# Kernel tuning notes

Measured on AMD Instinct MI355X. Metric: run time of the kernel, lower is better.

The kernel has to match this reference:

```python
import jax, jax.numpy as jnp
import numpy as np


def _layer_norm(x, g, b, eps=1e-5):
    mu = x.mean(-1, keepdims=True)
    var = ((x - mu) ** 2).mean(-1, keepdims=True)
    return (x - mu) * jax.lax.rsqrt(var + eps) * g + b


def _linear(x, w, b):
    # torch nn.Linear: y = x @ W^T + b, w has shape (out, in)
    return jnp.einsum('...i,oi->...o', x, w) + b


def setup_inputs() -> dict:
    key = jax.random.key(0)
    ks = jax.random.split(key, 12)
    B, N, C = 1, 512, 128
    s = 0.02  # weight init scale
    f32 = jnp.float32
    return {
        'X': jax.random.normal(ks[0], (B, N, N, C), f32),
        'mask': jax.random.randint(ks[1], (B, N, N, 1), 0, 2) > 0,
        # first LayerNorm
        'ln1_g': jnp.ones((C,), f32), 'ln1_b': jnp.zeros((C,), f32),
        # left edge MLP: Linear -> Sigmoid -> Linear
        'lw1': jax.random.normal(ks[2], (C, C), f32) * s, 'lb1': jnp.zeros((C,), f32),
        'lw2': jax.random.normal(ks[3], (C, C), f32) * s, 'lb2': jnp.zeros((C,), f32),
        # right edge MLP
        'rw1': jax.random.normal(ks[4], (C, C), f32) * s, 'rb1': jnp.zeros((C,), f32),
        'rw2': jax.random.normal(ks[5], (C, C), f32) * s, 'rb2': jnp.zeros((C,), f32),
        # skip gate: Linear -> Sigmoid
        'sw': jax.random.normal(ks[6], (C, C), f32) * s, 'sb': jnp.zeros((C,), f32),
        # combine: LayerNorm -> Linear
        'ln2_g': jnp.ones((C,), f32), 'ln2_b': jnp.zeros((C,), f32),
        'cw': jax.random.normal(ks[7], (C, C), f32) * s, 'cb': jnp.zeros((C,), f32),
    }


def reference(X, mask, ln1_g, ln1_b, lw1, lb1, lw2, lb2,
              rw1, rb1, rw2, rb2, sw, sb, ln2_g, ln2_b, cw, cb):
    h = _layer_norm(X, ln1_g, ln1_b)                      # (B,N,N,C)
    A = _linear(jax.nn.sigmoid(_linear(h, lw1, lb1)), lw2, lb2)
    Bm = _linear(jax.nn.sigmoid(_linear(h, rw1, rb1)), rw2, rb2)
    G = jax.nn.sigmoid(_linear(h, sw, sb))
    A = jnp.where(mask, A, 0.0)
    Bm = jnp.where(mask, Bm, 0.0)
    # triangle multiplication, 'outgoing': contract over k per channel
    T = jnp.einsum('bikc,bjkc->bijc', A, Bm)              # (B,N,N,C)
    Y = _linear(_layer_norm(T, ln2_g, ln2_b), cw, cb) * G
    return Y
```

## Files before the change

kernel.cpp:

```cpp
#include <hip/hip_runtime.h>

typedef unsigned short u16;
typedef unsigned int   u32;
typedef u32   u32x4  __attribute__((ext_vector_type(4)));
typedef __bf16 bf16x8 __attribute__((ext_vector_type(8)));
typedef float f32x4  __attribute__((ext_vector_type(4)));

#define NPOS (512*512)
#define WSLOT 16384

__device__ __forceinline__ u16 f2bf(float f){
  u32 u=__builtin_bit_cast(u32,f);
  u32 r=u+0x7fffu+((u>>16)&1u);
  return (u16)(r>>16);
}
__device__ __forceinline__ float bf2f(u16 s){ u32 u=((u32)s)<<16; return __builtin_bit_cast(float,u); }
union pk8 { u16 s[8]; u32x4 v; };

__device__ __forceinline__ bf16x8 cvt8(const float* p){
  f32x4 w0=*(const f32x4*)p, w1=*(const f32x4*)(p+4);
  bf16x8 b;
#pragma unroll
  for(int e=0;e<4;e++){ b[e]=(__bf16)w0[e]; b[4+e]=(__bf16)w1[e]; }
  return b;
}

__global__ __launch_bounds__(256) void k0(
    const float* __restrict__ lw1, const float* __restrict__ lw2,
    const float* __restrict__ rw1, const float* __restrict__ rw2,
    const float* __restrict__ sw,  const float* __restrict__ cw, u16* __restrict__ Wp)
{
  const float* srcs[6]={lw1,lw2,rw1,rw2,sw,cw};
  const float* W=srcs[blockIdx.x];
  u16* dst=Wp + (size_t)blockIdx.x*WSLOT;
  const int t=threadIdx.x, lane=t&63, wvv=t>>6, lr=lane&15, quad=lane>>4;
#pragma unroll
  for(int i=0;i<8;i++){
    int tile=wvv*8+i, nt=tile>>2, kk=tile&3;
    const float* p=W+(size_t)(nt*16+lr)*128+kk*32+quad*8;
    bf16x8 b=cvt8(p);
    *(u32x4*)(dst+((size_t)tile*64+lane)*8)=__builtin_bit_cast(u32x4,b);
  }
}

__device__ __forceinline__ void wave_gemm2(const u16 (*sh)[136], int wv, int lane,
    const u16* __restrict__ Wp, const float* __restrict__ bias, float o[4][2][4])
{
  const int lr=lane&15, quad=lane>>4;
  bf16x8 b[2][4];
#pragma unroll
  for(int n2=0;n2<2;n2++){
    const int nt=wv*2+n2;
#pragma unroll
    for(int kk=0;kk<4;kk++)
      b[n2][kk]=*(const bf16x8*)(Wp+((size_t)((nt*4+kk)*64+lane))*8);
  }
  float bv[2]={bias[(wv*2)*16+lr], bias[(wv*2+1)*16+lr]};
#pragma unroll
  for(int mt=0;mt<4;mt++){
    bf16x8 a[4];
#pragma unroll
    for(int kk=0;kk<4;kk++) a[kk]=*(const bf16x8*)&sh[mt*16+lr][kk*32+quad*8];
#pragma unroll
    for(int n2=0;n2<2;n2++){
      f32x4 acc={0.f,0.f,0.f,0.f};
#pragma unroll
      for(int kk=0;kk<4;kk++)
        acc=__builtin_amdgcn_mfma_f32_16x16x32_bf16(a[kk],b[n2][kk],acc,0,0,0);
#pragma unroll
      for(int r=0;r<4;r++) o[mt][n2][r]=acc[r]+bv[n2];
    }
  }
}

__device__ __forceinline__ void sig_to_lds2(u16 (*sh)[136], int wv,int lane, float o[4][2][4]){
  const int lr=lane&15, quad=lane>>4;
#pragma unroll
  for(int mt=0;mt<4;mt++)
#pragma unroll
    for(int n2=0;n2<2;n2++)
#pragma unroll
      for(int r=0;r<4;r++)
        sh[mt*16+quad*4+r][(wv*2+n2)*16+lr]=f2bf(1.f/(1.f+__expf(-o[mt][n2][r])));
}

__device__ __forceinline__ void mask_to_lds2(u16 (*sh)[136], int wv,int lane, float o[4][2][4], const float* smask){
  const int lr=lane&15, quad=lane>>4;
#pragma unroll
  for(int mt=0;mt<4;mt++)
#pragma unroll
    for(int n2=0;n2<2;n2++)
#pragma unroll
      for(int r=0;r<4;r++){
        int row=mt*16+quad*4+r;
        sh[row][(wv*2+n2)*16+lr]=f2bf(o[mt][n2][r]*smask[row]);
      }
}

__device__ __forceinline__ void store_tr(const u16 (*sh)[136], int t, u16* __restrict__ dst, int p0){
#pragma unroll
  for(int iter=0;iter<4;iter++){
    int c=iter*32+(t>>3);
    int pos=(t&7)*8;
    pk8 u;
#pragma unroll
    for(int r=0;r<8;r++){
      int rp=(r+(t>>3)+(t&7))&7;
      u.s[rp]=sh[pos+rp][c];
    }
    *(u32x4*)(dst+(size_t)c*NPOS+p0+pos)=u.v;
  }
}

__global__ __launch_bounds__(256,4) void k1(
    const float* __restrict__ X, const void* __restrict__ mask,
    const float* __restrict__ g1, const float* __restrict__ b1,
    const u16* __restrict__ Wp,
    const float* __restrict__ lb1, const float* __restrict__ lb2,
    const float* __restrict__ rb1, const float* __restrict__ rb2,
    const float* __restrict__ sb,
    u16* __restrict__ At, u16* __restrict__ Bt, float* __restrict__ G)
{
  __shared__ u16 shh[64][136];
  __shared__ u16 sht[64][136];
  __shared__ float smask[64];
  __shared__ int mpacked;
  const int t=threadIdx.x;
  const int p0=blockIdx.x*64;
  if(t==0){
    const int* m32=(const int*)mask;
    int pk=0;
#pragma unroll
    for(int i=0;i<32;i++){ u32 v=(u32)m32[i]; if(v>1u) pk=1; }
    mpacked=pk;
  }
  {
    int row=t>>2, q=t&3;
    const float* xp = X + (size_t)(p0+row)*128 + q*32;
    float v[32]; float s=0.f,s2=0.f;
#pragma unroll
    for(int u=0;u<8;u++){ f32x4 d=*(const f32x4*)(xp+u*4);
#pragma unroll
      for(int e=0;e<4;e++) v[u*4+e]=d[e]; }
#pragma unroll
    for(int i=0;i<32;i++){ s+=v[i]; s2+=v[i]*v[i]; }
    s+=__shfl_xor(s,1); s2+=__shfl_xor(s2,1);
    s+=__shfl_xor(s,2); s2+=__shfl_xor(s2,2);
    float mu=s*(1.f/128.f);
    float rstd=1.f/sqrtf(s2*(1.f/128.f)-mu*mu+1e-5f);
#pragma unroll
    for(int u=0;u<4;u++){
      pk8 o;
#pragma unroll
      for(int e=0;e<8;e++){
        int c=q*32+u*8+e;
        o.s[e]=f2bf((v[u*8+e]-mu)*rstd*g1[c]+b1[c]);
      }
      *(u32x4*)&shh[row][q*32+u*8]=o.v;
    }
  }
  __syncthreads();
  if(t<64){
    int p=p0+t;
    int mval = mpacked ? (int)((const unsigned char*)mask)[p] : ((const int*)mask)[p];
    smask[t]=(mval!=0)?1.f:0.f;
  }
  const int lane=t&63, wv=t>>6;
  float o[4][2][4];
  wave_gemm2(shh,wv,lane,Wp+0*WSLOT,lb1,o);
  sig_to_lds2(sht,wv,lane,o);
  __syncthreads();
  wave_gemm2(sht,wv,lane,Wp+1*WSLOT,lb2,o);
  __syncthreads();
  mask_to_lds2(sht,wv,lane,o,smask);
  __syncthreads();
  store_tr(sht,t,At,p0);
  wave_gemm2(shh,wv,lane,Wp+2*WSLOT,rb1,o);
  __syncthreads();
  sig_to_lds2(sht,wv,lane,o);
  __syncthreads();
  wave_gemm2(sht,wv,lane,Wp+3*WSLOT,rb2,o);
  __syncthreads();
  mask_to_lds2(sht,wv,lane,o,smask);
  __syncthreads();
  store_tr(sht,t,Bt,p0);
  wave_gemm2(shh,wv,lane,Wp+4*WSLOT,sb,o);
  const int lr=lane&15, quad=lane>>4;
#pragma unroll
  for(int mt=0;mt<4;mt++)
#pragma unroll
    for(int n2=0;n2<2;n2++)
#pragma unroll
      for(int r=0;r<4;r++){
        size_t p=p0+mt*16+quad*4+r;
        G[p*128+(wv*2+n2)*16+lr]=1.f/(1.f+__expf(-o[mt][n2][r]));
      }
}

__global__ __launch_bounds__(256) void k2(const u16* __restrict__ At, const u16* __restrict__ Bt,
                                          u16* __restrict__ T, int j_base, int jc)
{
  __shared__ u16 sA[128][72];
  __shared__ u16 sB[128][72];
  const int t=threadIdx.x, lane=t&63, wv=t>>6;
  const int c=blockIdx.z;
  const int i0=blockIdx.y*128;
  const int j0l=blockIdx.x*128;
  const int wm=(wv>>1)*64, wn=(wv&1)*64, lr=lane&15, quad=lane>>4;
  const u16* Ab = At + (size_t)c*NPOS + (size_t)i0*512;
  const u16* Bb = Bt + (size_t)c*NPOS + (size_t)(j_base+j0l)*512;
  f32x4 acc[4][4];
#pragma unroll
  for(int i=0;i<4;i++)
#pragma unroll
    for(int j=0;j<4;j++) acc[i][j]=(f32x4){0.f,0.f,0.f,0.f};
  for(int k0=0;k0<512;k0+=64){
#pragma unroll
    for(int it=0;it<4;it++){
      int idx=it*256+t, row=idx>>3, kp=idx&7;
      *(u32x4*)&sA[row][kp*8]=*(const u32x4*)(Ab+(size_t)row*512+k0+kp*8);
      *(u32x4*)&sB[row][kp*8]=*(const u32x4*)(Bb+(size_t)row*512+k0+kp*8);
    }
    __syncthreads();
#pragma unroll
    for(int ks=0;ks<2;ks++){
      bf16x8 a[4],b[4];
#pragma unroll
      for(int mt=0;mt<4;mt++) a[mt]=*(const bf16x8*)&sA[wm+mt*16+lr][ks*32+quad*8];
#pragma unroll
      for(int nt=0;nt<4;nt++) b[nt]=*(const bf16x8*)&sB[wn+nt*16+lr][ks*32+quad*8];
#pragma unroll
      for(int mt=0;mt<4;mt++)
#pragma unroll
        for(int nt=0;nt<4;nt++)
          acc[mt][nt]=__builtin_amdgcn_mfma_f32_16x16x32_bf16(a[mt],b[nt],acc[mt][nt],0,0,0);
    }
    __syncthreads();
  }
  u16* Tb = T + (size_t)c*512*jc;
#pragma unroll
  for(int mt=0;mt<4;mt++)
#pragma unroll
    for(int nt=0;nt<4;nt++)
#pragma unroll
      for(int r=0;r<4;r++){
        int row=i0+wm+mt*16+quad*4+r;
        int col=j0l+wn+nt*16+lr;
        Tb[(size_t)row*jc+col]=f2bf(acc[mt][nt][r]);
      }
}

__global__ __launch_bounds__(256) void k3(const u16* __restrict__ T,
    const u16* __restrict__ cwp,
    const float* __restrict__ g2, const float* __restrict__ b2,
    const float* __restrict__ cb, float* GY,
    int j_base, int jc, int jshift)
{
  __shared__ u16 sH[128][136];
  const int t=threadIdx.x;
  const int cp0=blockIdx.x*128;
  {
    int c=t>>1, half=t&1;
    const u16* Tp = T + (size_t)c*512*jc + cp0 + half*64;
#pragma unroll
    for(int u=0;u<8;u++){
      pk8 d; d.v=*(const u32x4*)(Tp+u*8);
#pragma unroll
      for(int e=0;e<8;e++) sH[half*64+u*8+e][c]=d.s[e];
    }
  }
  __syncthreads();
  {
    int pos=t>>1, half=t&1;
    float v[64]; float s=0.f,s2=0.f;
#pragma unroll
    for(int u=0;u<8;u++)
#pragma unroll
      for(int e=0;e<8;e++){ float x=bf2f(sH[pos][half*64+u*8+e]); v[u*8+e]=x; s+=x; s2+=x*x; }
    s+=__shfl_xor(s,1); s2+=__shfl_xor(s2,1);
    float mu=s*(1.f/128.f);
    float rstd=1.f/sqrtf(s2*(1.f/128.f)-mu*mu+1e-5f);
#pragma unroll
    for(int u=0;u<8;u++){
      pk8 o;
#pragma unroll
      for(int e=0;e<8;e++){
        int c=half*64+u*8+e;
        o.s[e]=f2bf((v[u*8+e]-mu)*rstd*g2[c]+b2[c]);
      }
      *(u32x4*)&sH[pos][half*64+u*8]=o.v;
    }
  }
  __syncthreads();
  const int lane=t&63, wv=t>>6, m0=wv*32, lr=lane&15, quad=lane>>4;
  bf16x8 a[2][4];
#pragma unroll
  for(int mt=0;mt<2;mt++)
#pragma unroll
    for(int kk=0;kk<4;kk++) a[mt][kk]=*(const bf16x8*)&sH[m0+mt*16+lr][kk*32+quad*8];
#pragma unroll
  for(int nt=0;nt<8;nt++){
    f32x4 a0={0.f,0.f,0.f,0.f}, a1={0.f,0.f,0.f,0.f};
#pragma unroll
    for(int kk=0;kk<4;kk++){
      bf16x8 b=*(const bf16x8*)(cwp+((size_t)((nt*4+kk)*64+lane))*8);
      a0=__builtin_amdgcn_mfma_f32_16x16x32_bf16(a[0][kk],b,a0,0,0,0);
      a1=__builtin_amdgcn_mfma_f32_16x16x32_bf16(a[1][kk],b,a1,0,0,0);
    }
    float cbv=cb[nt*16+lr];
#pragma unroll
    for(int mt=0;mt<2;mt++){
      f32x4 ac = mt? a1: a0;
#pragma unroll
      for(int r=0;r<4;r++){
        int l=m0+mt*16+quad*4+r;
        int pl=cp0+l;
        size_t p=((size_t)(pl>>jshift)<<9)+(size_t)j_base+(pl&(jc-1));
        int col=nt*16+lr;
        float gg=GY[p*128+col];
        GY[p*128+col]=(ac[r]+cbv)*gg;
      }
    }
  }
}

__global__ void kprobe(float* out, u32 wsmib){
  if(threadIdx.x==0 && blockIdx.x==0) out[0]=(float)wsmib;
}

extern "C" void kernel_launch(void* const* d_in, const int* in_sizes, int n_in,
                              void* d_out, int out_size, void* d_ws, size_t ws_size,
                              hipStream_t stream)
{
  (void)in_sizes; (void)n_in; (void)out_size;
  const float* X  =(const float*)d_in[0];
  const void*  mask=d_in[1];
  const float* g1 =(const float*)d_in[2];  const float* b1 =(const float*)d_in[3];
  const float* lw1=(const float*)d_in[4];  const float* lb1=(const float*)d_in[5];
  const float* lw2=(const float*)d_in[6];  const float* lb2=(const float*)d_in[7];
  const float* rw1=(const float*)d_in[8];  const float* rb1=(const float*)d_in[9];
  const float* rw2=(const float*)d_in[10]; const float* rb2=(const float*)d_in[11];
  const float* sw =(const float*)d_in[12]; const float* sb =(const float*)d_in[13];
  const float* g2 =(const float*)d_in[14]; const float* b2 =(const float*)d_in[15];
  const float* cw =(const float*)d_in[16]; const float* cb =(const float*)d_in[17];
  float* out=(float*)d_out;

  const size_t wbytes = (size_t)6*WSLOT*sizeof(u16);
  const size_t base = wbytes + 2*(size_t)NPOS*128*sizeof(u16);
  int jc=0, jshift=0;
  if      (ws_size >= base + (size_t)512*512*128*2){ jc=512; jshift=9; }
  else if (ws_size >= base + (size_t)512*256*128*2){ jc=256; jshift=8; }
  else if (ws_size >= base + (size_t)512*128*128*2){ jc=128; jshift=7; }
  if(jc==0){
    kprobe<<<dim3(1),dim3(64),0,stream>>>(out,(u32)(ws_size>>20));
    return;
  }
  u16* Wp=(u16*)d_ws;
  u16* At=Wp+(size_t)6*WSLOT;
  u16* Bt=At+(size_t)NPOS*128;
  u16* T =Bt+(size_t)NPOS*128;

  k0<<<dim3(6),dim3(256),0,stream>>>(lw1,lw2,rw1,rw2,sw,cw,Wp);
  k1<<<dim3(4096),dim3(256),0,stream>>>(X,mask,g1,b1,Wp,lb1,lb2,rb1,rb2,sb,At,Bt,out);
  for(int jb=0;jb<512;jb+=jc){
    k2<<<dim3(jc/128,4,128),dim3(256),0,stream>>>(At,Bt,T,jb,jc);
    k3<<<dim3(4*jc),dim3(256),0,stream>>>(T,Wp+(size_t)5*WSLOT,g2,b2,cb,out,jb,jc,jshift);
  }
}
```

Measured before the change: 527.2 us.

## Load k2 tiles directly to LDS with XOR swizzle and interleave left/right MLPs

The triangle GEMM kernel k2 now uses global_load_lds 16-byte direct-to-LDS loads into an unpadded, XOR-swizzled shared layout. This removes the register round trip and keeps LDS reads free of bank conflicts. In k1 the left and right edge MLPs now run interleaved with separate LDS buffers, which halves the barriers and exposes more independent MFMA work, at the cost of more LDS and registers (occupancy hint lowered from 4 to 3). The bf16 conversion now uses the native cast instead of manual rounding.

```diff
diff --git a/kernel.cpp b/kernel.cpp
--- a/kernel.cpp
+++ b/kernel.cpp
@@ -10,12 +10,16 @@
 #define WSLOT 16384
 
 __device__ __forceinline__ u16 f2bf(float f){
-  u32 u=__builtin_bit_cast(u32,f);
-  u32 r=u+0x7fffu+((u>>16)&1u);
-  return (u16)(r>>16);
+  __bf16 h=(__bf16)f;
+  return __builtin_bit_cast(u16,h);
 }
 __device__ __forceinline__ float bf2f(u16 s){ u32 u=((u32)s)<<16; return __builtin_bit_cast(float,u); }
 union pk8 { u16 s[8]; u32x4 v; };
+
+__device__ __forceinline__ void gload16(const void* g, void* l){
+  __builtin_amdgcn_global_load_lds((const __attribute__((address_space(1))) void*)g,
+                                   (__attribute__((address_space(3))) void*)l, 16, 0, 0);
+}
 
 __device__ __forceinline__ bf16x8 cvt8(const float* p){
   f32x4 w0=*(const f32x4*)p, w1=*(const f32x4*)(p+4);
@@ -112,7 +116,7 @@
   }
 }
 
-__global__ __launch_bounds__(256,4) void k1(
+__global__ __launch_bounds__(256,3) void k1(
     const float* __restrict__ X, const void* __restrict__ mask,
     const float* __restrict__ g1, const float* __restrict__ b1,
     const u16* __restrict__ Wp,
@@ -121,8 +125,9 @@
     const float* __restrict__ sb,
     u16* __restrict__ At, u16* __restrict__ Bt, float* __restrict__ G)
 {
-  __shared__ u16 shh[64][136];
-  __shared__ u16 sht[64][136];
+  __shared__ u16 shh [64][136];
+  __shared__ u16 shtL[64][136];
+  __shared__ u16 shtR[64][136];
   __shared__ float smask[64];
   __shared__ int mpacked;
   const int t=threadIdx.x;
@@ -166,25 +171,21 @@
     smask[t]=(mval!=0)?1.f:0.f;
   }
   const int lane=t&63, wv=t>>6;
-  float o[4][2][4];
-  wave_gemm2(shh,wv,lane,Wp+0*WSLOT,lb1,o);
-  sig_to_lds2(sht,wv,lane,o);
-  __syncthreads();
-  wave_gemm2(sht,wv,lane,Wp+1*WSLOT,lb2,o);
-  __syncthreads();
-  mask_to_lds2(sht,wv,lane,o,smask);
-  __syncthreads();
-  store_tr(sht,t,At,p0);
-  wave_gemm2(shh,wv,lane,Wp+2*WSLOT,rb1,o);
-  __syncthreads();
-  sig_to_lds2(sht,wv,lane,o);
-  __syncthreads();
-  wave_gemm2(sht,wv,lane,Wp+3*WSLOT,rb2,o);
-  __syncthreads();
-  mask_to_lds2(sht,wv,lane,o,smask);
-  __syncthreads();
-  store_tr(sht,t,Bt,p0);
-  wave_gemm2(shh,wv,lane,Wp+4*WSLOT,sb,o);
+  float oL[4][2][4], oR[4][2][4];
+  wave_gemm2(shh,wv,lane,Wp+0*WSLOT,lb1,oL);
+  wave_gemm2(shh,wv,lane,Wp+2*WSLOT,rb1,oR);
+  sig_to_lds2(shtL,wv,lane,oL);
+  sig_to_lds2(shtR,wv,lane,oR);
+  __syncthreads();
+  wave_gemm2(shtL,wv,lane,Wp+1*WSLOT,lb2,oL);
+  wave_gemm2(shtR,wv,lane,Wp+3*WSLOT,rb2,oR);
+  __syncthreads();
+  mask_to_lds2(shtL,wv,lane,oL,smask);
+  mask_to_lds2(shtR,wv,lane,oR,smask);
+  __syncthreads();
+  store_tr(shtL,t,At,p0);
+  store_tr(shtR,t,Bt,p0);
+  wave_gemm2(shh,wv,lane,Wp+4*WSLOT,sb,oL);
   const int lr=lane&15, quad=lane>>4;
 #pragma unroll
   for(int mt=0;mt<4;mt++)
@@ -193,15 +194,15 @@
 #pragma unroll
       for(int r=0;r<4;r++){
         size_t p=p0+mt*16+quad*4+r;
-        G[p*128+(wv*2+n2)*16+lr]=1.f/(1.f+__expf(-o[mt][n2][r]));
+        G[p*128+(wv*2+n2)*16+lr]=1.f/(1.f+__expf(-oL[mt][n2][r]));
       }
 }
 
 __global__ __launch_bounds__(256) void k2(const u16* __restrict__ At, const u16* __restrict__ Bt,
                                           u16* __restrict__ T, int j_base, int jc)
 {
-  __shared__ u16 sA[128][72];
-  __shared__ u16 sB[128][72];
+  __shared__ u16 sA[128*64];
+  __shared__ u16 sB[128*64];
   const int t=threadIdx.x, lane=t&63, wv=t>>6;
   const int c=blockIdx.z;
   const int i0=blockIdx.y*128;
@@ -209,6 +210,9 @@
   const int wm=(wv>>1)*64, wn=(wv&1)*64, lr=lane&15, quad=lane>>4;
   const u16* Ab = At + (size_t)c*NPOS + (size_t)i0*512;
   const u16* Bb = Bt + (size_t)c*NPOS + (size_t)(j_base+j0l)*512;
+  const int srow = lane>>3;
+  const int scol = ((lane&7) ^ srow)*8;
+  const int swz  = (lr&7)<<4;
   f32x4 acc[4][4];
 #pragma unroll
   for(int i=0;i<4;i++)
@@ -216,19 +220,28 @@
     for(int j=0;j<4;j++) acc[i][j]=(f32x4){0.f,0.f,0.f,0.f};
   for(int k0=0;k0<512;k0+=64){
 #pragma unroll
-    for(int it=0;it<4;it++){
-      int idx=it*256+t, row=idx>>3, kp=idx&7;
-      *(u32x4*)&sA[row][kp*8]=*(const u32x4*)(Ab+(size_t)row*512+k0+kp*8);
-      *(u32x4*)&sB[row][kp*8]=*(const u32x4*)(Bb+(size_t)row*512+k0+kp*8);
+    for(int j=0;j<4;j++){
+      int seg=wv*4+j;
+      int row=seg*8+srow;
+      gload16(Ab + (size_t)row*512 + k0 + scol, &sA[seg*512]);
+      gload16(Bb + (size_t)row*512 + k0 + scol, &sB[seg*512]);
     }
     __syncthreads();
+    const char* sAc=(const char*)sA;
+    const char* sBc=(const char*)sB;
 #pragma unroll
     for(int ks=0;ks<2;ks++){
       bf16x8 a[4],b[4];
 #pragma unroll
-      for(int mt=0;mt<4;mt++) a[mt]=*(const bf16x8*)&sA[wm+mt*16+lr][ks*32+quad*8];
-#pragma unroll
-      for(int nt=0;nt<4;nt++) b[nt]=*(const bf16x8*)&sB[wn+nt*16+lr][ks*32+quad*8];
+      for(int mt=0;mt<4;mt++){
+        int row=wm+mt*16+lr;
+        a[mt]=*(const bf16x8*)(sAc + row*128 + ((ks*64+quad*16)^swz));
+      }
+#pragma unroll
+      for(int nt=0;nt<4;nt++){
+        int row=wn+nt*16+lr;
+        b[nt]=*(const bf16x8*)(sBc + row*128 + ((ks*64+quad*16)^swz));
+      }
 #pragma unroll
       for(int mt=0;mt<4;mt++)
 #pragma unroll
```

After: 548.1 us. 1.04x slower.
